# Optimization experiments

Hardware: AMD Instinct MI355X
Metric: run time of the kernel (lower is better)

Reference implementation:

```python
import jax, jax.numpy as jnp
import numpy as np

B = 8          # batch size (static)
GRID = 1024    # spatial grid H = W
PER = 25000    # active sites per batch item
N = B * PER

_OFFSETS = [(dx, dy) for dx in (-1, 0, 1) for dy in (-1, 0, 1)]  # 3x3 kernel


def _build_sparse_inputs():
    """Sample unique active 2D coords per batch item and build the 3x3
    submanifold neighbor map: nbr[i, k] = index of neighbor site at kernel
    offset k, or -1 if that coordinate is inactive."""
    rng = np.random.default_rng(0)
    bs, xs, ys = [], [], []
    for b in range(B):
        flat = rng.choice(GRID * GRID, size=PER, replace=False)
        bs.append(np.full(PER, b, np.int64))
        xs.append((flat // GRID).astype(np.int64))
        ys.append((flat % GRID).astype(np.int64))
    bb = np.concatenate(bs); xx = np.concatenate(xs); yy = np.concatenate(ys)
    # hash lookup table: (b, x, y) -> site index
    lut = np.full(B * GRID * GRID, -1, np.int64)
    lut[bb * GRID * GRID + xx * GRID + yy] = np.arange(N, dtype=np.int64)
    nbr = np.full((N, 9), -1, np.int64)
    for k, (dx, dy) in enumerate(_OFFSETS):
        nx, ny = xx + dx, yy + dy
        ok = (nx >= 0) & (nx < GRID) & (ny >= 0) & (ny < GRID)
        key = bb * GRID * GRID + np.clip(nx, 0, GRID - 1) * GRID + np.clip(ny, 0, GRID - 1)
        nbr[:, k] = np.where(ok, lut[key], -1)
    return bb, nbr


def setup_inputs() -> dict:
    key = jax.random.key(0)
    k1, k2, k3 = jax.random.split(key, 3)
    batch_np, nbr_np = _build_sparse_inputs()
    feats = jax.random.normal(k1, (N, 3), dtype=jnp.float32)
    # He (kaiming normal, relu): std = sqrt(2 / fan_in), fan_in = 9 * Cin
    W1 = jax.random.normal(k2, (9, 3, 256), dtype=jnp.float32) * np.sqrt(2.0 / (9 * 3))
    W2 = jax.random.normal(k3, (9, 256, 256), dtype=jnp.float32) * np.sqrt(2.0 / (9 * 256))
    return {
        "feats": feats,
        "W1": W1,
        "W2": W2,
        "nbr": jnp.asarray(nbr_np),
        "batch_ids": jnp.asarray(batch_np),
    }


def _subm_conv(feat, W, nbr):
    """Submanifold 3x3 conv: out[i] = sum_k feat[nbr[i,k]] @ W[k] over valid
    neighbors. feat: [N, Cin], W: [9, Cin, Cout], nbr: [N, 9] -> [N, Cout]."""
    out = jnp.zeros((feat.shape[0], W.shape[2]), dtype=feat.dtype)
    for k in range(9):  # fixed small kernel loop
        idx = nbr[:, k]
        valid = (idx >= 0).astype(feat.dtype)[:, None]
        g = feat[jnp.maximum(idx, 0)] * valid  # masked gather [N, Cin]
        out = out + g @ W[k]
    return out


def reference(feats, W1, W2, nbr, batch_ids):
    h = jax.nn.relu(_subm_conv(feats, W1, nbr))   # [N, 256]
    h = jax.nn.relu(_subm_conv(h, W2, nbr))       # [N, 256]
    # global average pool per batch item -> [B, 256]
    sums = jax.ops.segment_sum(h, batch_ids, num_segments=B)
    counts = jax.ops.segment_sum(jnp.ones((h.shape[0],), h.dtype), batch_ids, num_segments=B)
    return sums / counts[:, None]
```

## Files before the change

kernel.cpp:

```cpp
#include <hip/hip_runtime.h>
#include <hip/hip_bf16.h>

typedef __attribute__((ext_vector_type(8))) short bh8;
typedef __attribute__((ext_vector_type(4))) float f32x4;

#define NB 8
#define SLOTS 64
#define CAP 6144
#define CROWS 36864
#define CBLOCKS 512
#define FROWS 64
#define TSTRIDE 264

__device__ __forceinline__ void gld_lds16(const void* g, void* l) {
  __builtin_amdgcn_global_load_lds(
      (const __attribute__((address_space(1))) void*)g,
      (__attribute__((address_space(3))) void*)l, 16, 0, 0);
}

__device__ __forceinline__ unsigned short f2bu(float f) {
  union { __hip_bfloat16 h; unsigned short u; } cv;
  cv.h = __float2bfloat16(f);
  return cv.u;
}
__device__ __forceinline__ float bu2f(unsigned short u) {
  return __uint_as_float(((unsigned)u) << 16);
}

__global__ void w1t_kernel(const float* __restrict__ W1, short* __restrict__ w1bt) {
  const int n = threadIdx.x;
#pragma unroll
  for (int kk = 0; kk < 32; ++kk)
    w1bt[n * 32 + kk] = (kk < 27) ? (short)f2bu(W1[kk * 256 + n]) : (short)0;
}

__device__ __forceinline__ float3 ldf3(const float* __restrict__ f,
                                       const int* s_nbr, int idx) {
  int s = s_nbr[idx];
  long long sc = (s < 0) ? 0 : s;
  float3 r;
  r.x = f[3 * sc]; r.y = f[3 * sc + 1]; r.z = f[3 * sc + 2];
  if (s < 0) { r.x = 0.f; r.y = 0.f; r.z = 0.f; }
  return r;
}

__global__ __launch_bounds__(256, 2) void conv1_mfma_kernel(
    const float* __restrict__ feats, const short* __restrict__ w1bt,
    const int* __restrict__ nbr, __hip_bfloat16* __restrict__ h1b, int N) {
  __shared__ int s_nbr[64 * 9];
  __shared__ unsigned short tile[64 * TSTRIDE];
  const int tid = threadIdx.x;
  const int base = blockIdx.x * 64;

  for (int t = tid; t < 64 * 9; t += 256) s_nbr[t] = nbr[base * 9 + t];
  __syncthreads();

  const int wave = tid >> 6, lane = tid & 63;
  const int q = lane >> 4, m16 = lane & 15;
  const int rbase = (wave * 16 + m16) * 9;

  bh8 a;
  if (q == 0) {
    float3 t0 = ldf3(feats, s_nbr, rbase + 0);
    float3 t1 = ldf3(feats, s_nbr, rbase + 1);
    float3 t2 = ldf3(feats, s_nbr, rbase + 2);
    a[0] = (short)f2bu(t0.x); a[1] = (short)f2bu(t0.y); a[2] = (short)f2bu(t0.z);
    a[3] = (short)f2bu(t1.x); a[4] = (short)f2bu(t1.y); a[5] = (short)f2bu(t1.z);
    a[6] = (short)f2bu(t2.x); a[7] = (short)f2bu(t2.y);
  } else if (q == 1) {
    float3 t2 = ldf3(feats, s_nbr, rbase + 2);
    float3 t3 = ldf3(feats, s_nbr, rbase + 3);
    float3 t4 = ldf3(feats, s_nbr, rbase + 4);
    float3 t5 = ldf3(feats, s_nbr, rbase + 5);
    a[0] = (short)f2bu(t2.z);
    a[1] = (short)f2bu(t3.x); a[2] = (short)f2bu(t3.y); a[3] = (short)f2bu(t3.z);
    a[4] = (short)f2bu(t4.x); a[5] = (short)f2bu(t4.y); a[6] = (short)f2bu(t4.z);
    a[7] = (short)f2bu(t5.x);
  } else if (q == 2) {
    float3 t5 = ldf3(feats, s_nbr, rbase + 5);
    float3 t6 = ldf3(feats, s_nbr, rbase + 6);
    float3 t7 = ldf3(feats, s_nbr, rbase + 7);
    a[0] = (short)f2bu(t5.y); a[1] = (short)f2bu(t5.z);
    a[2] = (short)f2bu(t6.x); a[3] = (short)f2bu(t6.y); a[4] = (short)f2bu(t6.z);
    a[5] = (short)f2bu(t7.x); a[6] = (short)f2bu(t7.y); a[7] = (short)f2bu(t7.z);
  } else {
    float3 t8 = ldf3(feats, s_nbr, rbase + 8);
    a[0] = (short)f2bu(t8.x); a[1] = (short)f2bu(t8.y); a[2] = (short)f2bu(t8.z);
    a[3] = 0; a[4] = 0; a[5] = 0; a[6] = 0; a[7] = 0;
  }

  f32x4 acc[16];
#pragma unroll
  for (int nj = 0; nj < 16; ++nj) {
    bh8 b = *(const bh8*)(w1bt + (nj * 16 + m16) * 32 + q * 8);
    acc[nj] = __builtin_amdgcn_mfma_f32_16x16x32_bf16(a, b, (f32x4)0.f, 0, 0, 0);
  }

#pragma unroll
  for (int nj = 0; nj < 16; ++nj)
#pragma unroll
    for (int rr = 0; rr < 4; ++rr)
      tile[(wave * 16 + q * 4 + rr) * TSTRIDE + nj * 16 + m16] =
          f2bu(fmaxf(acc[nj][rr], 0.f));
  __syncthreads();

  {
    const int row = tid >> 2, seg = tid & 3;
    const int4* src = (const int4*)&tile[row * TSTRIDE + seg * 64];
    int4* dst = (int4*)(h1b + (long long)(base + row) * 256 + seg * 64);
#pragma unroll
    for (int i = 0; i < 8; ++i) dst[i] = src[i];
  }
}

__global__ __launch_bounds__(256) void w2t_kernel(
    const float* __restrict__ W2, __hip_bfloat16* __restrict__ w2bt) {
  __shared__ float tile[16][256];
  int k = blockIdx.x >> 4, t = blockIdx.x & 15;
  int tid = threadIdx.x;
#pragma unroll
  for (int r = 0; r < 16; ++r) tile[r][tid] = W2[k * 65536 + (t * 16 + r) * 256 + tid];
  __syncthreads();
#pragma unroll
  for (int r = 0; r < 16; ++r)
    w2bt[k * 65536 + tid * 256 + t * 16 + r] = __float2bfloat16(tile[r][tid]);
}

__global__ __launch_bounds__(256) void build_pairs_kernel(
    const int* __restrict__ nbr, const int* __restrict__ bid,
    int* __restrict__ nOff, int* __restrict__ cnt, float* __restrict__ bcnt,
    int* __restrict__ cidmap, int* __restrict__ crow,
    int* __restrict__ psrc, int* __restrict__ pcnt_cid,
    int* __restrict__ pairlist, int N) {
  __shared__ int l_cnt[10];
  __shared__ int l_base[10];
  __shared__ int l_bcnt[NB];
  const int tid = threadIdx.x;
  if (tid < 10) l_cnt[tid] = 0;
  if (tid < NB) l_bcnt[tid] = 0;
  __syncthreads();

  const int i = blockIdx.x * 256 + tid;
  const bool active = (i < N);
  int s[9];
  int kpos[9];
  int loc_cid = -1;
  if (active) {
#pragma unroll
    for (int k = 0; k < 9; ++k) s[k] = nbr[i * 9 + k];
    bool any = false;
#pragma unroll
    for (int k = 0; k < 9; ++k)
      if (k != 4 && s[k] >= 0) any = true;
    if (any) {
      loc_cid = atomicAdd(&l_cnt[9], 1);
#pragma unroll
      for (int k = 0; k < 9; ++k) {
        kpos[k] = -1;
        if (k != 4 && s[k] >= 0) kpos[k] = atomicAdd(&l_cnt[k], 1);
      }
    }
    atomicAdd(&l_bcnt[bid[i]], 1);
  }
  __syncthreads();

  if (tid < 9) l_base[tid] = (l_cnt[tid] > 0) ? atomicAdd(&cnt[tid], l_cnt[tid]) : 0;
  else if (tid == 9) l_base[9] = (l_cnt[9] > 0) ? atomicAdd(nOff, l_cnt[9]) : 0;
  if (tid >= 32 && tid < 32 + NB && l_bcnt[tid - 32] > 0)
    atomicAdd(&bcnt[tid - 32], (float)l_bcnt[tid - 32]);
  __syncthreads();

  if (active) {
    int cid = -1;
    if (loc_cid >= 0) {
      cid = l_base[9] + loc_cid;
      if (cid >= CROWS) cid = -1;
    }
    cidmap[i] = cid;
    if (cid >= 0) {
      crow[cid] = i;
#pragma unroll
      for (int k = 0; k < 9; ++k) {
        if (k == 4 || kpos[k] < 0 || s[k] < 0) continue;
        int pos = l_base[k] + kpos[k];
        if (pos < CAP) {
          psrc[k * CAP + pos] = s[k];
          int slot = atomicAdd(&pcnt_cid[cid], 1);
          if (slot < 8) pairlist[cid * 8 + slot] = k * CAP + pos;
        }
      }
    }
  }
}

__global__ __launch_bounds__(256, 2) void off_gemm_kernel(
    const __hip_bfloat16* __restrict__ h1, const __hip_bfloat16* __restrict__ w2bt,
    const int* __restrict__ cnt, const int* __restrict__ psrc,
    unsigned short* __restrict__ pout) {
  const int bpk = CAP / 64;
  int koff = blockIdx.x / bpk;
  int grp = blockIdx.x - koff * bpk;
  int k = koff + (koff >= 4 ? 1 : 0);
  int cntk = cnt[k];
  const int base = grp * 64;
  if (base >= cntk) return;

  __shared__ int s_src[64];
  const int tid = threadIdx.x;
  if (tid < 64) {
    int m = base + tid;
    s_src[tid] = (m < cntk) ? psrc[k * CAP + m] : 0;
  }

  const int wave = tid >> 6, lane = tid & 63, q = lane >> 4, m16 = lane & 15;
  const short* h1s = (const short*)h1;
  const short* wts = (const short*)w2bt + k * 65536;

  bh8 breg[4][8];
#pragma unroll
  for (int nj = 0; nj < 4; ++nj)
#pragma unroll
    for (int ko = 0; ko < 8; ++ko)
      breg[nj][ko] = *(const bh8*)(wts + (wave * 64 + nj * 16 + m16) * 256 + ko * 32 + q * 8);
  __syncthreads();

  bh8 aA[8];
  {
    const short* ap = h1s + (long long)s_src[m16] * 256 + q * 8;
#pragma unroll
    for (int ko = 0; ko < 8; ++ko) aA[ko] = *(const bh8*)(ap + ko * 32);
  }

#pragma unroll
  for (int t = 0; t < 4; ++t) {
    bh8 aN[8];
    if (t < 3) {
      const short* ap = h1s + (long long)s_src[(t + 1) * 16 + m16] * 256 + q * 8;
#pragma unroll
      for (int ko = 0; ko < 8; ++ko) aN[ko] = *(const bh8*)(ap + ko * 32);
    }
    f32x4 acc[4];
#pragma unroll
    for (int ko = 0; ko < 8; ++ko)
#pragma unroll
      for (int nj = 0; nj < 4; ++nj)
        acc[nj] = __builtin_amdgcn_mfma_f32_16x16x32_bf16(
            aA[ko], breg[nj][ko], (ko == 0) ? (f32x4)0.f : acc[nj], 0, 0, 0);
#pragma unroll
    for (int r = 0; r < 4; ++r) {
      int m = base + t * 16 + q * 4 + r;
      if (m >= cntk) continue;
      const long long rowb = (long long)(k * CAP + m) * 256;
#pragma unroll
      for (int nj = 0; nj < 4; ++nj)
        pout[rowb + wave * 64 + nj * 16 + m16] = f2bu(acc[nj][r]);
    }
#pragma unroll
    for (int ko = 0; ko < 8; ++ko) aA[ko] = aN[ko];
    if (base + (t + 1) * 16 >= cntk) break;
  }
}

__global__ __launch_bounds__(512, 2) void center_gemm_kernel(
    const __hip_bfloat16* __restrict__ h1, const __hip_bfloat16* __restrict__ w2bt,
    const int* __restrict__ cidmap, const int* __restrict__ bid,
    float* __restrict__ psums, unsigned short* __restrict__ h2cb, int N) {
  __shared__ __align__(16) short Abuf[2][64 * 256];

  const int tid = threadIdx.x;
  const int wave = tid >> 6, lane = tid & 63;
  const int q = lane >> 4, m16 = lane & 15;
  const int wc = wave << 5;
  const int slot = blockIdx.x & (SLOTS - 1);

  const short* h1s = (const short*)h1;
  const short* wts = (const short*)w2bt + 4 * 65536;

  bh8 breg[2][8];
#pragma unroll
  for (int nj = 0; nj < 2; ++nj)
#pragma unroll
    for (int ko = 0; ko < 8; ++ko)
      breg[nj][ko] = *(const bh8*)(wts + (wc + nj * 16 + m16) * 256 + ko * 32 + q * 8);

  const int nchunk = (N + 63) >> 6;
  const int span = (nchunk + CBLOCKS - 1) / CBLOCKS;
  const int c0 = blockIdx.x * span;
  if (c0 >= nchunk) return;
  int c1 = c0 + span;
  if (c1 > nchunk) c1 = nchunk;

  const int lrow = lane >> 5;
  const int jch  = lane & 31;

#define STAGE_CHUNK(cc, b)                                                     \
  {                                                                            \
    _Pragma("unroll") for (int t = 0; t < 4; ++t) {                            \
      int lr = (wave << 3) + (t << 1) + lrow;                                  \
      int g = ((cc) << 6) + lr;                                                \
      if (g >= N) g = N - 1;                                                   \
      int js = jch ^ (lr & 31);                                                \
      const short* src = h1s + (long long)g * 256 + (js << 3);                 \
      short* dst = &Abuf[b][((wave << 3) + (t << 1)) << 8];                    \
      gld_lds16((const void*)src, (void*)dst);                                 \
    }                                                                          \
  }

#define FLUSH_SACC()                                                           \
  if (cur_b0 >= 0) {                                                           \
    _Pragma("unroll") for (int lb = 0; lb < 2; ++lb) {                         \
      _Pragma("unroll") for (int nj = 0; nj < 2; ++nj) {                       \
        float v = sacc[lb][nj];                                                \
        v += __shfl_xor(v, 16, 64);                                            \
        v += __shfl_xor(v, 32, 64);                                            \
        if (q == 0 && v != 0.f) {                                              \
          int b = cur_b0 + lb;                                                 \
          if (b < NB)                                                          \
            atomicAdd(&psums[(slot * NB + b) * 256 + wc + nj * 16 + m16], v);  \
        }                                                                      \
      }                                                                        \
    }                                                                          \
  }

  STAGE_CHUNK(c0, 0);
  int cur = 0;
  int cur_b0 = -1;
  float sacc[2][2];
#pragma unroll
  for (int lb = 0; lb < 2; ++lb)
#pragma unroll
    for (int nj = 0; nj < 2; ++nj) sacc[lb][nj] = 0.f;

  for (int c = c0; c < c1; ++c) {
    __syncthreads();

    int4 bid4[4], cid4[4];
#pragma unroll
    for (int mi = 0; mi < 4; ++mi) {
      const int rb = (c << 6) + mi * 16 + q * 4;
      bid4[mi] = *(const int4*)(&bid[rb]);
      cid4[mi] = *(const int4*)(&cidmap[rb]);
    }
    const int b0 = bid[c << 6];

    if (c + 1 < c1) STAGE_CHUNK(c + 1, cur ^ 1);

    const short* Ab = &Abuf[cur][0];
    const short* abase[4];
    int xr[4];
#pragma unroll
    for (int mi = 0; mi < 4; ++mi) {
      int R = mi * 16 + m16;
      xr[mi] = R & 31;
      abase[mi] = Ab + (R << 8);
    }

    f32x4 acc[4][2];
#pragma unroll
    for (int ko = 0; ko < 8; ++ko) {
      bh8 a[4];
#pragma unroll
      for (int mi = 0; mi < 4; ++mi)
        a[mi] = *(const bh8*)(abase[mi] + (((ko * 4 + q) ^ xr[mi]) << 3));
#pragma unroll
      for (int mi = 0; mi < 4; ++mi)
#pragma unroll
        for (int nj = 0; nj < 2; ++nj)
          acc[mi][nj] = __builtin_amdgcn_mfma_f32_16x16x32_bf16(
              a[mi], breg[nj][ko], (ko == 0) ? (f32x4)0.f : acc[mi][nj], 0, 0, 0);
    }

    if (b0 != cur_b0) {
      FLUSH_SACC();
#pragma unroll
      for (int lb = 0; lb < 2; ++lb)
#pragma unroll
        for (int nj = 0; nj < 2; ++nj) sacc[lb][nj] = 0.f;
      cur_b0 = b0;
    }
#pragma unroll
    for (int mi = 0; mi < 4; ++mi) {
      const int bb[4] = {bid4[mi].x, bid4[mi].y, bid4[mi].z, bid4[mi].w};
      const int cc4[4] = {cid4[mi].x, cid4[mi].y, cid4[mi].z, cid4[mi].w};
      const int rb = (c << 6) + mi * 16 + q * 4;
#pragma unroll
      for (int rr = 0; rr < 4; ++rr) {
        if (rb + rr >= N) continue;
        if (cc4[rr] >= 0) {
          unsigned short* hp = h2cb + (long long)cc4[rr] * 256 + wc + m16;
          hp[0] = f2bu(acc[mi][0][rr]);
          hp[16] = f2bu(acc[mi][1][rr]);
          continue;
        }
        const int lb = (bb[rr] != b0) ? 1 : 0;
#pragma unroll
        for (int nj = 0; nj < 2; ++nj)
          sacc[lb][nj] += fmaxf(acc[mi][nj][rr], 0.f);
      }
    }

    cur ^= 1;
  }
  FLUSH_SACC();
#undef STAGE_CHUNK
#undef FLUSH_SACC
}

__global__ __launch_bounds__(256) void fixup_kernel(
    const unsigned short* __restrict__ h2cb, const unsigned short* __restrict__ pout,
    const int* __restrict__ pairlist, const int* __restrict__ pcnt_cid,
    const int* __restrict__ crow, const int* __restrict__ bid,
    const int* __restrict__ nOffp, float* __restrict__ psums) {
  __shared__ float lsum[NB * 256];
  __shared__ int s_b[FROWS], s_np[FROWS], s_pl[FROWS * 8];
  int nc = *nOffp;
  if (nc > CROWS) nc = CROWS;
  const int t0 = blockIdx.x * FROWS;
  if (t0 >= nc) return;
  const int tid = threadIdx.x;

  if (tid < FROWS) {
    int m = t0 + tid;
    bool v = (m < nc);
    s_b[tid] = v ? bid[crow[m]] : -1;
    int np = v ? pcnt_cid[m] : 0;
    s_np[tid] = (np > 8) ? 8 : np;
  }
  for (int i = tid; i < FROWS * 8; i += 256) {
    int m = t0 + (i >> 3);
    s_pl[i] = (m < nc) ? pairlist[m * 8 + (i & 7)] : 0;
  }
#pragma unroll
  for (int b = 0; b < NB; ++b) lsum[b * 256 + tid] = 0.f;
  __syncthreads();

  const int g = tid >> 6;
  const int cg = tid & 63;
  const ushort4* h2v = (const ushort4*)h2cb;
  const ushort4* pov = (const ushort4*)pout;

  float4 s0 = {0.f, 0.f, 0.f, 0.f}, s1 = {0.f, 0.f, 0.f, 0.f};
  const int r0 = g * 16;
  const int b0 = s_b[r0];
  int b1 = -1;
  for (int r = r0; r < r0 + 16; ++r) {
    const int b = s_b[r];
    if (b < 0) break;
    ushort4 u = h2v[(long long)(t0 + r) * 64 + cg];
    float4 x = {bu2f(u.x), bu2f(u.y), bu2f(u.z), bu2f(u.w)};
    const int np = s_np[r];
    for (int j = 0; j < np; ++j) {
      ushort4 p = pov[(long long)s_pl[r * 8 + j] * 64 + cg];
      x.x += bu2f(p.x); x.y += bu2f(p.y); x.z += bu2f(p.z); x.w += bu2f(p.w);
    }
    x.x = fmaxf(x.x, 0.f); x.y = fmaxf(x.y, 0.f);
    x.z = fmaxf(x.z, 0.f); x.w = fmaxf(x.w, 0.f);
    if (b == b0) {
      s0.x += x.x; s0.y += x.y; s0.z += x.z; s0.w += x.w;
    } else {
      b1 = b;
      s1.x += x.x; s1.y += x.y; s1.z += x.z; s1.w += x.w;
    }
  }
  if (b0 >= 0) {
    float* p0 = &lsum[b0 * 256 + cg * 4];
    atomicAdd(p0 + 0, s0.x); atomicAdd(p0 + 1, s0.y);
    atomicAdd(p0 + 2, s0.z); atomicAdd(p0 + 3, s0.w);
  }
  if (b1 >= 0 && b1 < NB) {
    float* p1 = &lsum[b1 * 256 + cg * 4];
    atomicAdd(p1 + 0, s1.x); atomicAdd(p1 + 1, s1.y);
    atomicAdd(p1 + 2, s1.z); atomicAdd(p1 + 3, s1.w);
  }
  __syncthreads();

  const int slot = blockIdx.x & (SLOTS - 1);
#pragma unroll
  for (int b = 0; b < NB; ++b) {
    float v = lsum[b * 256 + tid];
    if (v != 0.f) atomicAdd(&psums[(slot * NB + b) * 256 + tid], v);
  }
}

__global__ void finalize_kernel(const float* __restrict__ psums,
                                const float* __restrict__ bcnt,
                                float* __restrict__ out) {
  int b = blockIdx.x, c = threadIdx.x;
  float s = 0.f;
  for (int t = 0; t < SLOTS; ++t) s += psums[(t * NB + b) * 256 + c];
  out[b * 256 + c] = s / bcnt[b];
}

extern "C" void kernel_launch(void* const* d_in, const int* in_sizes, int n_in,
                              void* d_out, int out_size, void* d_ws, size_t ws_size,
                              hipStream_t stream) {
  const float* feats = (const float*)d_in[0];
  const float* W1    = (const float*)d_in[1];
  const float* W2    = (const float*)d_in[2];
  const int*   nbr   = (const int*)d_in[3];
  const int*   bid   = (const int*)d_in[4];
  float* out = (float*)d_out;
  const int N = in_sizes[0] / 3;

  char* ws = (char*)d_ws;
  size_t o = 0;
  float* psums = (float*)(ws + o); o += (size_t)SLOTS * NB * 256 * 4;
  float* bcnt  = (float*)(ws + o); o += NB * 4;
  int*   nOff  = (int*)(ws + o);   o += 4;
  int*   cnt   = (int*)(ws + o);   o += 9 * 4;
  o = (o + 255) & ~(size_t)255;
  int* pcnt_cid = (int*)(ws + o); o += (size_t)CROWS * 4;
  size_t zero1 = o;
  int* psrc = (int*)(ws + o); o += (size_t)9 * CAP * 4;
  int* pairlist = (int*)(ws + o); o += (size_t)CROWS * 8 * 4;
  int* cidmap = (int*)(ws + o); o += (size_t)N * 4;
  int* crow = (int*)(ws + o); o += (size_t)CROWS * 4;
  o = (o + 255) & ~(size_t)255;
  unsigned short* h2cb = (unsigned short*)(ws + o); o += (size_t)CROWS * 256 * 2;
  unsigned short* pout = (unsigned short*)(ws + o); o += (size_t)9 * CAP * 256 * 2;
  __hip_bfloat16* w2bt = (__hip_bfloat16*)(ws + o); o += (size_t)9 * 65536 * 2;
  short* w1bt = (short*)(ws + o); o += (size_t)256 * 32 * 2;
  __hip_bfloat16* h1b  = (__hip_bfloat16*)(ws + o); o += (size_t)N * 256 * 2;

  hipMemsetAsync(d_ws, 0, zero1, stream);

  w1t_kernel<<<1, 256, 0, stream>>>(W1, w1bt);
  conv1_mfma_kernel<<<(N + 63) / 64, 256, 0, stream>>>(feats, w1bt, nbr, h1b, N);
  w2t_kernel<<<9 * 16, 256, 0, stream>>>(W2, w2bt);
  build_pairs_kernel<<<(N + 255) / 256, 256, 0, stream>>>(
      nbr, bid, nOff, cnt, bcnt, cidmap, crow, psrc, pcnt_cid, pairlist, N);
  off_gemm_kernel<<<8 * (CAP / 64), 256, 0, stream>>>(h1b, w2bt, cnt, psrc, pout);
  center_gemm_kernel<<<CBLOCKS, 512, 0, stream>>>(h1b, w2bt, cidmap, bid, psums,
                                                  h2cb, N);
  fixup_kernel<<<(CROWS + FROWS - 1) / FROWS, 256, 0, stream>>>(
      h2cb, pout, pairlist, pcnt_cid, crow, bid, nOff, psums);
  finalize_kernel<<<NB, 256, 0, stream>>>(psums, bcnt, out);
}
```

Before: 271.6 us.

## Merge preprocessing and GEMM kernels into two heterogeneous phase kernels

Merges w1 transpose, conv1, w2 transpose and pair building into one phase1 kernel whose blocks pick their role from the block index, and merges the center and offset GEMMs into one phase2 kernel. Center rows that need fixup now get their center product from a separate gathered GEMM over crow instead of being written during the dense pass. Each conv1 block now converts W1 into LDS itself, and conv1 writes h1 directly without LDS staging. The goal is fewer launches and better overlap of the small kernels, at the cost of redundant W1 conversion, uncoalesced h1 stores, and a grid of mixed block types with different resource needs.

New measurement: 272.1 us. About the same (+0.2%).

```diff
diff --git a/kernel.cpp b/kernel.cpp
--- a/kernel.cpp
+++ b/kernel.cpp
@@ -8,9 +8,8 @@
 #define SLOTS 64
 #define CAP 6144
 #define CROWS 36864
-#define CBLOCKS 512
+#define CGB 256
 #define FROWS 64
-#define TSTRIDE 264
 
 __device__ __forceinline__ void gld_lds16(const void* g, void* l) {
   __builtin_amdgcn_global_load_lds(
@@ -27,271 +26,186 @@
   return __uint_as_float(((unsigned)u) << 16);
 }
 
-__global__ void w1t_kernel(const float* __restrict__ W1, short* __restrict__ w1bt) {
-  const int n = threadIdx.x;
-#pragma unroll
-  for (int kk = 0; kk < 32; ++kk)
-    w1bt[n * 32 + kk] = (kk < 27) ? (short)f2bu(W1[kk * 256 + n]) : (short)0;
-}
-
-__device__ __forceinline__ float3 ldf3(const float* __restrict__ f,
-                                       const int* s_nbr, int idx) {
-  int s = s_nbr[idx];
-  long long sc = (s < 0) ? 0 : s;
-  float3 r;
-  r.x = f[3 * sc]; r.y = f[3 * sc + 1]; r.z = f[3 * sc + 2];
-  if (s < 0) { r.x = 0.f; r.y = 0.f; r.z = 0.f; }
-  return r;
-}
-
-__global__ __launch_bounds__(256, 2) void conv1_mfma_kernel(
-    const float* __restrict__ feats, const short* __restrict__ w1bt,
-    const int* __restrict__ nbr, __hip_bfloat16* __restrict__ h1b, int N) {
-  __shared__ int s_nbr[64 * 9];
-  __shared__ unsigned short tile[64 * TSTRIDE];
+__global__ __launch_bounds__(256, 2) void phase1_kernel(
+    const float* __restrict__ feats, const float* __restrict__ W1,
+    const float* __restrict__ W2, const int* __restrict__ nbr,
+    const int* __restrict__ bid, __hip_bfloat16* __restrict__ h1b,
+    __hip_bfloat16* __restrict__ w2bt, int* __restrict__ nOff,
+    int* __restrict__ cnt, float* __restrict__ bcnt, int* __restrict__ cidmap,
+    int* __restrict__ crow, int* __restrict__ psrc, int* __restrict__ pcnt_cid,
+    int* __restrict__ pairlist, int N) {
+  __shared__ union {
+    struct { unsigned short w1s[256 * 32]; int s_nbr[64 * 9]; } c1;
+    struct { int l_cnt[10]; int l_base[10]; int l_bcnt[NB]; } bld;
+    struct { float tile[16][256]; } w2;
+  } sm;
+
+  const int nc1 = (N + 63) >> 6;
+  const int nbld = (N + 255) >> 8;
+  int bx = blockIdx.x;
   const int tid = threadIdx.x;
-  const int base = blockIdx.x * 64;
-
-  for (int t = tid; t < 64 * 9; t += 256) s_nbr[t] = nbr[base * 9 + t];
-  __syncthreads();
-
-  const int wave = tid >> 6, lane = tid & 63;
-  const int q = lane >> 4, m16 = lane & 15;
-  const int rbase = (wave * 16 + m16) * 9;
-
-  bh8 a;
-  if (q == 0) {
-    float3 t0 = ldf3(feats, s_nbr, rbase + 0);
-    float3 t1 = ldf3(feats, s_nbr, rbase + 1);
-    float3 t2 = ldf3(feats, s_nbr, rbase + 2);
-    a[0] = (short)f2bu(t0.x); a[1] = (short)f2bu(t0.y); a[2] = (short)f2bu(t0.z);
-    a[3] = (short)f2bu(t1.x); a[4] = (short)f2bu(t1.y); a[5] = (short)f2bu(t1.z);
-    a[6] = (short)f2bu(t2.x); a[7] = (short)f2bu(t2.y);
-  } else if (q == 1) {
-    float3 t2 = ldf3(feats, s_nbr, rbase + 2);
-    float3 t3 = ldf3(feats, s_nbr, rbase + 3);
-    float3 t4 = ldf3(feats, s_nbr, rbase + 4);
-    float3 t5 = ldf3(feats, s_nbr, rbase + 5);
-    a[0] = (short)f2bu(t2.z);
-    a[1] = (short)f2bu(t3.x); a[2] = (short)f2bu(t3.y); a[3] = (short)f2bu(t3.z);
-    a[4] = (short)f2bu(t4.x); a[5] = (short)f2bu(t4.y); a[6] = (short)f2bu(t4.z);
-    a[7] = (short)f2bu(t5.x);
-  } else if (q == 2) {
-    float3 t5 = ldf3(feats, s_nbr, rbase + 5);
-    float3 t6 = ldf3(feats, s_nbr, rbase + 6);
-    float3 t7 = ldf3(feats, s_nbr, rbase + 7);
-    a[0] = (short)f2bu(t5.y); a[1] = (short)f2bu(t5.z);
-    a[2] = (short)f2bu(t6.x); a[3] = (short)f2bu(t6.y); a[4] = (short)f2bu(t6.z);
-    a[5] = (short)f2bu(t7.x); a[6] = (short)f2bu(t7.y); a[7] = (short)f2bu(t7.z);
-  } else {
-    float3 t8 = ldf3(feats, s_nbr, rbase + 8);
-    a[0] = (short)f2bu(t8.x); a[1] = (short)f2bu(t8.y); a[2] = (short)f2bu(t8.z);
-    a[3] = 0; a[4] = 0; a[5] = 0; a[6] = 0; a[7] = 0;
-  }
-
-  f32x4 acc[16];
-#pragma unroll
-  for (int nj = 0; nj < 16; ++nj) {
-    bh8 b = *(const bh8*)(w1bt + (nj * 16 + m16) * 32 + q * 8);
-    acc[nj] = __builtin_amdgcn_mfma_f32_16x16x32_bf16(a, b, (f32x4)0.f, 0, 0, 0);
-  }
-
-#pragma unroll
-  for (int nj = 0; nj < 16; ++nj)
-#pragma unroll
-    for (int rr = 0; rr < 4; ++rr)
-      tile[(wave * 16 + q * 4 + rr) * TSTRIDE + nj * 16 + m16] =
-          f2bu(fmaxf(acc[nj][rr], 0.f));
-  __syncthreads();
+
+  if (bx < nc1) {
+    const int base = bx * 64;
+#pragma unroll 9
+    for (int kk = 0; kk < 27; ++kk)
+      sm.c1.w1s[tid * 32 + kk] = f2bu(W1[kk * 256 + tid]);
+#pragma unroll
+    for (int kk = 27; kk < 32; ++kk) sm.c1.w1s[tid * 32 + kk] = 0;
+    for (int t = tid; t < 64 * 9; t += 256) sm.c1.s_nbr[t] = nbr[base * 9 + t];
+    __syncthreads();
+
+    const int wave = tid >> 6, lane = tid & 63;
+    const int q = lane >> 4, m16 = lane & 15;
+    const int rbase = (wave * 16 + m16) * 9;
+    const int* s_nbr = sm.c1.s_nbr;
+
+    float v[9 * 3];
+    int t_lo[4] = {0, 2, 5, 8}, t_hi[4] = {3, 6, 8, 9};
+    for (int tt = t_lo[q]; tt < t_hi[q]; ++tt) {
+      int s = s_nbr[rbase + tt];
+      long long sc = (s < 0) ? 0 : s;
+      float x = feats[3 * sc], y = feats[3 * sc + 1], z = feats[3 * sc + 2];
+      if (s < 0) { x = 0.f; y = 0.f; z = 0.f; }
+      v[tt * 3 + 0] = x; v[tt * 3 + 1] = y; v[tt * 3 + 2] = z;
+    }
+    bh8 a;
+#pragma unroll
+    for (int j = 0; j < 8; ++j) {
+      int col = q * 8 + j;
+      a[j] = (col < 27) ? (short)f2bu(v[col]) : (short)0;
+    }
+
+    f32x4 acc[16];
+#pragma unroll
+    for (int nj = 0; nj < 16; ++nj) {
+      bh8 b = *(const bh8*)(&sm.c1.w1s[(nj * 16 + m16) * 32 + q * 8]);
+      acc[nj] = __builtin_amdgcn_mfma_f32_16x16x32_bf16(a, b, (f32x4)0.f, 0, 0, 0);
+    }
+    const int growb = base + wave * 16 + q * 4;
+#pragma unroll
+    for (int rr = 0; rr < 4; ++rr) {
+      __hip_bfloat16* rowp = h1b + (long long)(growb + rr) * 256 + m16;
+#pragma unroll
+      for (int nj = 0; nj < 16; ++nj)
+        rowp[nj * 16] = __float2bfloat16(fmaxf(acc[nj][rr], 0.f));
+    }
+    return;
+  }
+  bx -= nc1;
+
+  if (bx < nbld) {
+    if (tid < 10) sm.bld.l_cnt[tid] = 0;
+    if (tid < NB) sm.bld.l_bcnt[tid] = 0;
+    __syncthreads();
+
+    const int i = bx * 256 + tid;
+    const bool active = (i < N);
+    int s[9];
+    int kpos[9];
+    int loc_cid = -1;
+    if (active) {
+#pragma unroll
+      for (int k = 0; k < 9; ++k) s[k] = nbr[i * 9 + k];
+      bool any = false;
+#pragma unroll
+      for (int k = 0; k < 9; ++k)
+        if (k != 4 && s[k] >= 0) any = true;
+      if (any) {
+        loc_cid = atomicAdd(&sm.bld.l_cnt[9], 1);
+#pragma unroll
+        for (int k = 0; k < 9; ++k) {
+          kpos[k] = -1;
+          if (k != 4 && s[k] >= 0) kpos[k] = atomicAdd(&sm.bld.l_cnt[k], 1);
+        }
+      }
+      atomicAdd(&sm.bld.l_bcnt[bid[i]], 1);
+    }
+    __syncthreads();
+
+    if (tid < 9)
+      sm.bld.l_base[tid] =
+          (sm.bld.l_cnt[tid] > 0) ? atomicAdd(&cnt[tid], sm.bld.l_cnt[tid]) : 0;
+    else if (tid == 9)
+      sm.bld.l_base[9] = (sm.bld.l_cnt[9] > 0) ? atomicAdd(nOff, sm.bld.l_cnt[9]) : 0;
+    if (tid >= 32 && tid < 32 + NB && sm.bld.l_bcnt[tid - 32] > 0)
+      atomicAdd(&bcnt[tid - 32], (float)sm.bld.l_bcnt[tid - 32]);
+    __syncthreads();
+
+    if (active) {
+      int cid = -1;
+      if (loc_cid >= 0) {
+        cid = sm.bld.l_base[9] + loc_cid;
+        if (cid >= CROWS) cid = -1;
+      }
+      cidmap[i] = cid;
+      if (cid >= 0) {
+        crow[cid] = i;
+#pragma unroll
+        for (int k = 0; k < 9; ++k) {
+          if (k == 4 || kpos[k] < 0 || s[k] < 0) continue;
+          int pos = sm.bld.l_base[k] + kpos[k];
+          if (pos < CAP) {
+            psrc[k * CAP + pos] = s[k];
+            int slot = atomicAdd(&pcnt_cid[cid], 1);
+            if (slot < 8) pairlist[cid * 8 + slot] = k * CAP + pos;
+          }
+        }
+      }
+    }
+    return;
+  }
+  bx -= nbld;
 
   {
-    const int row = tid >> 2, seg = tid & 3;
-    const int4* src = (const int4*)&tile[row * TSTRIDE + seg * 64];
-    int4* dst = (int4*)(h1b + (long long)(base + row) * 256 + seg * 64);
-#pragma unroll
-    for (int i = 0; i < 8; ++i) dst[i] = src[i];
-  }
-}
-
-__global__ __launch_bounds__(256) void w2t_kernel(
-    const float* __restrict__ W2, __hip_bfloat16* __restrict__ w2bt) {
-  __shared__ float tile[16][256];
-  int k = blockIdx.x >> 4, t = blockIdx.x & 15;
-  int tid = threadIdx.x;
-#pragma unroll
-  for (int r = 0; r < 16; ++r) tile[r][tid] = W2[k * 65536 + (t * 16 + r) * 256 + tid];
-  __syncthreads();
-#pragma unroll
-  for (int r = 0; r < 16; ++r)
-    w2bt[k * 65536 + tid * 256 + t * 16 + r] = __float2bfloat16(tile[r][tid]);
-}
-
-__global__ __launch_bounds__(256) void build_pairs_kernel(
-    const int* __restrict__ nbr, const int* __restrict__ bid,
-    int* __restrict__ nOff, int* __restrict__ cnt, float* __restrict__ bcnt,
-    int* __restrict__ cidmap, int* __restrict__ crow,
-    int* __restrict__ psrc, int* __restrict__ pcnt_cid,
-    int* __restrict__ pairlist, int N) {
-  __shared__ int l_cnt[10];
-  __shared__ int l_base[10];
-  __shared__ int l_bcnt[NB];
-  const int tid = threadIdx.x;
-  if (tid < 10) l_cnt[tid] = 0;
-  if (tid < NB) l_bcnt[tid] = 0;
-  __syncthreads();
-
-  const int i = blockIdx.x * 256 + tid;
-  const bool active = (i < N);
-  int s[9];
-  int kpos[9];
-  int loc_cid = -1;
-  if (active) {
-#pragma unroll
-    for (int k = 0; k < 9; ++k) s[k] = nbr[i * 9 + k];
-    bool any = false;
-#pragma unroll
-    for (int k = 0; k < 9; ++k)
-      if (k != 4 && s[k] >= 0) any = true;
-    if (any) {
-      loc_cid = atomicAdd(&l_cnt[9], 1);
-#pragma unroll
-      for (int k = 0; k < 9; ++k) {
-        kpos[k] = -1;
-        if (k != 4 && s[k] >= 0) kpos[k] = atomicAdd(&l_cnt[k], 1);
-      }
-    }
-    atomicAdd(&l_bcnt[bid[i]], 1);
-  }
-  __syncthreads();
-
-  if (tid < 9) l_base[tid] = (l_cnt[tid] > 0) ? atomicAdd(&cnt[tid], l_cnt[tid]) : 0;
-  else if (tid == 9) l_base[9] = (l_cnt[9] > 0) ? atomicAdd(nOff, l_cnt[9]) : 0;
-  if (tid >= 32 && tid < 32 + NB && l_bcnt[tid - 32] > 0)
-    atomicAdd(&bcnt[tid - 32], (float)l_bcnt[tid - 32]);
-  __syncthreads();
-
-  if (active) {
-    int cid = -1;
-    if (loc_cid >= 0) {
-      cid = l_base[9] + loc_cid;
-      if (cid >= CROWS) cid = -1;
-    }
-    cidmap[i] = cid;
-    if (cid >= 0) {
-      crow[cid] = i;
-#pragma unroll
-      for (int k = 0; k < 9; ++k) {
-        if (k == 4 || kpos[k] < 0 || s[k] < 0) continue;
-        int pos = l_base[k] + kpos[k];
-        if (pos < CAP) {
-          psrc[k * CAP + pos] = s[k];
-          int slot = atomicAdd(&pcnt_cid[cid], 1);
-          if (slot < 8) pairlist[cid * 8 + slot] = k * CAP + pos;
-        }
-      }
-    }
-  }
-}
-
-__global__ __launch_bounds__(256, 2) void off_gemm_kernel(
-    const __hip_bfloat16* __restrict__ h1, const __hip_bfloat16* __restrict__ w2bt,
-    const int* __restrict__ cnt, const int* __restrict__ psrc,
-    unsigned short* __restrict__ pout) {
-  const int bpk = CAP / 64;
-  int koff = blockIdx.x / bpk;
-  int grp = blockIdx.x - koff * bpk;
-  int k = koff + (koff >= 4 ? 1 : 0);
-  int cntk = cnt[k];
-  const int base = grp * 64;
-  if (base >= cntk) return;
-
-  __shared__ int s_src[64];
-  const int tid = threadIdx.x;
-  if (tid < 64) {
-    int m = base + tid;
-    s_src[tid] = (m < cntk) ? psrc[k * CAP + m] : 0;
-  }
-
-  const int wave = tid >> 6, lane = tid & 63, q = lane >> 4, m16 = lane & 15;
-  const short* h1s = (const short*)h1;
-  const short* wts = (const short*)w2bt + k * 65536;
-
-  bh8 breg[4][8];
-#pragma unroll
-  for (int nj = 0; nj < 4; ++nj)
-#pragma unroll
-    for (int ko = 0; ko < 8; ++ko)
-      breg[nj][ko] = *(const bh8*)(wts + (wave * 64 + nj * 16 + m16) * 256 + ko * 32 + q * 8);
-  __syncthreads();
-
-  bh8 aA[8];
-  {
-    const short* ap = h1s + (long long)s_src[m16] * 256 + q * 8;
-#pragma unroll
-    for (int ko = 0; ko < 8; ++ko) aA[ko] = *(const bh8*)(ap + ko * 32);
-  }
-
-#pragma unroll
-  for (int t = 0; t < 4; ++t) {
-    bh8 aN[8];
-    if (t < 3) {
-      const short* ap = h1s + (long long)s_src[(t + 1) * 16 + m16] * 256 + q * 8;
-#pragma unroll
-      for (int ko = 0; ko < 8; ++ko) aN[ko] = *(const bh8*)(ap + ko * 32);
-    }
-    f32x4 acc[4];
-#pragma unroll
-    for (int ko = 0; ko < 8; ++ko)
-#pragma unroll
-      for (int nj = 0; nj < 4; ++nj)
-        acc[nj] = __builtin_amdgcn_mfma_f32_16x16x32_bf16(
-            aA[ko], breg[nj][ko], (ko == 0) ? (f32x4)0.f : acc[nj], 0, 0, 0);
-#pragma unroll
-    for (int r = 0; r < 4; ++r) {
-      int m = base + t * 16 + q * 4 + r;
-      if (m >= cntk) continue;
-      const long long rowb = (long long)(k * CAP + m) * 256;
-#pragma unroll
-      for (int nj = 0; nj < 4; ++nj)
-        pout[rowb + wave * 64 + nj * 16 + m16] = f2bu(acc[nj][r]);
-    }
-#pragma unroll
-    for (int ko = 0; ko < 8; ++ko) aA[ko] = aN[ko];
-    if (base + (t + 1) * 16 >= cntk) break;
-  }
-}
-
-__global__ __launch_bounds__(512, 2) void center_gemm_kernel(
+    int k = bx >> 4, t = bx & 15;
+#pragma unroll
+    for (int r = 0; r < 16; ++r)
+      sm.w2.tile[r][tid] = W2[k * 65536 + (t * 16 + r) * 256 + tid];
+    __syncthreads();
+#pragma unroll
+    for (int r = 0; r < 16; ++r)
+      w2bt[k * 65536 + tid * 256 + t * 16 + r] = __float2bfloat16(sm.w2.tile[r][tid]);
+  }
+}
+
+__global__ __launch_bounds__(512, 2) void phase2_kernel(
     const __hip_bfloat16* __restrict__ h1, const __hip_bfloat16* __restrict__ w2bt,
     const int* __restrict__ cidmap, const int* __restrict__ bid,
-    float* __restrict__ psums, unsigned short* __restrict__ h2cb, int N) {
+    const int* __restrict__ cnt, const int* __restrict__ psrc,
+    const int* __restrict__ nOffp, const int* __restrict__ crow,
+    float* __restrict__ psums, unsigned short* __restrict__ h2cb,
+    unsigned short* __restrict__ pout, int N) {
   __shared__ __align__(16) short Abuf[2][64 * 256];
 
+  int bx = blockIdx.x;
   const int tid = threadIdx.x;
   const int wave = tid >> 6, lane = tid & 63;
   const int q = lane >> 4, m16 = lane & 15;
-  const int wc = wave << 5;
-  const int slot = blockIdx.x & (SLOTS - 1);
-
   const short* h1s = (const short*)h1;
-  const short* wts = (const short*)w2bt + 4 * 65536;
-
-  bh8 breg[2][8];
-#pragma unroll
-  for (int nj = 0; nj < 2; ++nj)
-#pragma unroll
-    for (int ko = 0; ko < 8; ++ko)
-      breg[nj][ko] = *(const bh8*)(wts + (wc + nj * 16 + m16) * 256 + ko * 32 + q * 8);
-
-  const int nchunk = (N + 63) >> 6;
-  const int span = (nchunk + CBLOCKS - 1) / CBLOCKS;
-  const int c0 = blockIdx.x * span;
-  if (c0 >= nchunk) return;
-  int c1 = c0 + span;
-  if (c1 > nchunk) c1 = nchunk;
-
-  const int lrow = lane >> 5;
-  const int jch  = lane & 31;
+
+  if (bx < CGB) {
+    const int wc = wave << 5;
+    const int slot = bx & (SLOTS - 1);
+    const short* wts = (const short*)w2bt + 4 * 65536;
+
+    bh8 breg[2][8];
+#pragma unroll
+    for (int nj = 0; nj < 2; ++nj)
+#pragma unroll
+      for (int ko = 0; ko < 8; ++ko)
+        breg[nj][ko] =
+            *(const bh8*)(wts + (wc + nj * 16 + m16) * 256 + ko * 32 + q * 8);
+
+    const int nchunk = (N + 63) >> 6;
+    const int span = (nchunk + CGB - 1) / CGB;
+    const int c0 = bx * span;
+    if (c0 >= nchunk) return;
+    int c1 = c0 + span;
+    if (c1 > nchunk) c1 = nchunk;
+
+    const int lrow = lane >> 5;
+    const int jch = lane & 31;
 
 #define STAGE_CHUNK(cc, b)                                                     \
   {                                                                            \
@@ -322,88 +236,147 @@
     }                                                                          \
   }
 
-  STAGE_CHUNK(c0, 0);
-  int cur = 0;
-  int cur_b0 = -1;
-  float sacc[2][2];
-#pragma unroll
-  for (int lb = 0; lb < 2; ++lb)
-#pragma unroll
-    for (int nj = 0; nj < 2; ++nj) sacc[lb][nj] = 0.f;
-
-  for (int c = c0; c < c1; ++c) {
-    __syncthreads();
-
-    int4 bid4[4], cid4[4];
-#pragma unroll
-    for (int mi = 0; mi < 4; ++mi) {
-      const int rb = (c << 6) + mi * 16 + q * 4;
-      bid4[mi] = *(const int4*)(&bid[rb]);
-      cid4[mi] = *(const int4*)(&cidmap[rb]);
-    }
-    const int b0 = bid[c << 6];
-
-    if (c + 1 < c1) STAGE_CHUNK(c + 1, cur ^ 1);
-
-    const short* Ab = &Abuf[cur][0];
-    const short* abase[4];
-    int xr[4];
-#pragma unroll
-    for (int mi = 0; mi < 4; ++mi) {
-      int R = mi * 16 + m16;
-      xr[mi] = R & 31;
-      abase[mi] = Ab + (R << 8);
-    }
-
-    f32x4 acc[4][2];
-#pragma unroll
-    for (int ko = 0; ko < 8; ++ko) {
-      bh8 a[4];
-#pragma unroll
-      for (int mi = 0; mi < 4; ++mi)
-        a[mi] = *(const bh8*)(abase[mi] + (((ko * 4 + q) ^ xr[mi]) << 3));
-#pragma unroll
-      for (int mi = 0; mi < 4; ++mi)
-#pragma unroll
-        for (int nj = 0; nj < 2; ++nj)
-          acc[mi][nj] = __builtin_amdgcn_mfma_f32_16x16x32_bf16(
-              a[mi], breg[nj][ko], (ko == 0) ? (f32x4)0.f : acc[mi][nj], 0, 0, 0);
-    }
-
-    if (b0 != cur_b0) {
-      FLUSH_SACC();
-#pragma unroll
-      for (int lb = 0; lb < 2; ++lb)
-#pragma unroll
-        for (int nj = 0; nj < 2; ++nj) sacc[lb][nj] = 0.f;
-      cur_b0 = b0;
-    }
-#pragma unroll
-    for (int mi = 0; mi < 4; ++mi) {
-      const int bb[4] = {bid4[mi].x, bid4[mi].y, bid4[mi].z, bid4[mi].w};
-      const int cc4[4] = {cid4[mi].x, cid4[mi].y, cid4[mi].z, cid4[mi].w};
-      const int rb = (c << 6) + mi * 16 + q * 4;
-#pragma unroll
-      for (int rr = 0; rr < 4; ++rr) {
-        if (rb + rr >= N) continue;
-        if (cc4[rr] >= 0) {
-          unsigned short* hp = h2cb + (long long)cc4[rr] * 256 + wc + m16;
-          hp[0] = f2bu(acc[mi][0][rr]);
-          hp[16] = f2bu(acc[mi][1][rr]);
-          continue;
+    STAGE_CHUNK(c0, 0);
+    int cur = 0;
+    int cur_b0 = -1;
+    float sacc[2][2];
+#pragma unroll
+    for (int lb = 0; lb < 2; ++lb)
+#pragma unroll
+      for (int nj = 0; nj < 2; ++nj) sacc[lb][nj] = 0.f;
+
+    for (int c = c0; c < c1; ++c) {
+      __syncthreads();
+
+      int4 bid4[4], cid4[4];
+#pragma unroll
+      for (int mi = 0; mi < 4; ++mi) {
+        const int rb = (c << 6) + mi * 16 + q * 4;
+        bid4[mi] = *(const int4*)(&bid[rb]);
+        cid4[mi] = *(const int4*)(&cidmap[rb]);
+      }
+      const int b0 = bid[c << 6];
+
+      if (c + 1 < c1) STAGE_CHUNK(c + 1, cur ^ 1);
+
+      const short* Ab = &Abuf[cur][0];
+      const short* abase[4];
+      int xr[4];
+#pragma unroll
+      for (int mi = 0; mi < 4; ++mi) {
+        int R = mi * 16 + m16;
+        xr[mi] = R & 31;
+        abase[mi] = Ab + (R << 8);
+      }
+
+      f32x4 acc[4][2];
+#pragma unroll
+      for (int ko = 0; ko < 8; ++ko) {
+        bh8 a[4];
+#pragma unroll
+        for (int mi = 0; mi < 4; ++mi)
+          a[mi] = *(const bh8*)(abase[mi] + (((ko * 4 + q) ^ xr[mi]) << 3));
+#pragma unroll
+        for (int mi = 0; mi < 4; ++mi)
+#pragma unroll
+          for (int nj = 0; nj < 2; ++nj)
+            acc[mi][nj] = __builtin_amdgcn_mfma_f32_16x16x32_bf16(
+                a[mi], breg[nj][ko], (ko == 0) ? (f32x4)0.f : acc[mi][nj], 0, 0, 0);
+      }
+
+      if (b0 != cur_b0) {
+        FLUSH_SACC();
+#pragma unroll
+        for (int lb = 0; lb < 2; ++lb)
+#pragma unroll
+          for (int nj = 0; nj < 2; ++nj) sacc[lb][nj] = 0.f;
+        cur_b0 = b0;
+      }
+#pragma unroll
+      for (int mi = 0; mi < 4; ++mi) {
+        const int bb[4] = {bid4[mi].x, bid4[mi].y, bid4[mi].z, bid4[mi].w};
+        const int cc4[4] = {cid4[mi].x, cid4[mi].y, cid4[mi].z, cid4[mi].w};
+        const int rb = (c << 6) + mi * 16 + q * 4;
+#pragma unroll
+        for (int rr = 0; rr < 4; ++rr) {
+          if (rb + rr >= N) continue;
+          if (cc4[rr] >= 0) continue;
+          const int lb = (bb[rr] != b0) ? 1 : 0;
+#pragma unroll
+          for (int nj = 0; nj < 2; ++nj)
+            sacc[lb][nj] += fmaxf(acc[mi][nj][rr], 0.f);
         }
-        const int lb = (bb[rr] != b0) ? 1 : 0;
-#pragma unroll
-        for (int nj = 0; nj < 2; ++nj)
-          sacc[lb][nj] += fmaxf(acc[mi][nj][rr], 0.f);
-      }
-    }
-
-    cur ^= 1;
-  }
-  FLUSH_SACC();
+      }
+      cur ^= 1;
+    }
+    FLUSH_SACC();
 #undef STAGE_CHUNK
 #undef FLUSH_SACC
+    return;
+  }
+  bx -= CGB;
+
+  int* s_src = (int*)&Abuf[0][0];
+  const int OFFG = 8 * (CAP / 64);
+  int k = 4;
+  int gbase, cmax;
+  bool isoff;
+  if (bx < OFFG) {
+    int koff = bx / (CAP / 64);
+    int grp = bx - koff * (CAP / 64);
+    k = koff + (koff >= 4 ? 1 : 0);
+    cmax = cnt[k];
+    gbase = grp * 64;
+    isoff = true;
+  } else {
+    bx -= OFFG;
+    cmax = *nOffp;
+    if (cmax > CROWS) cmax = CROWS;
+    gbase = bx * 64;
+    isoff = false;
+  }
+  if (gbase >= cmax) return;
+
+  if (tid < 64) {
+    int m = gbase + tid;
+    s_src[tid] = (m < cmax) ? (isoff ? psrc[k * CAP + m] : crow[m]) : 0;
+  }
+  const short* wts = (const short*)w2bt + k * 65536;
+  const int wc = wave << 5;
+
+  bh8 breg[2][8];
+#pragma unroll
+  for (int nj = 0; nj < 2; ++nj)
+#pragma unroll
+    for (int ko = 0; ko < 8; ++ko)
+      breg[nj][ko] = *(const bh8*)(wts + (wc + nj * 16 + m16) * 256 + ko * 32 + q * 8);
+  __syncthreads();
+
+  for (int t = 0; t < 4; ++t) {
+    if (gbase + t * 16 >= cmax) break;
+    bh8 aA[8];
+    {
+      const short* ap = h1s + (long long)s_src[t * 16 + m16] * 256 + q * 8;
+#pragma unroll
+      for (int ko = 0; ko < 8; ++ko) aA[ko] = *(const bh8*)(ap + ko * 32);
+    }
+    f32x4 acc[2];
+#pragma unroll
+    for (int ko = 0; ko < 8; ++ko)
+#pragma unroll
+      for (int nj = 0; nj < 2; ++nj)
+        acc[nj] = __builtin_amdgcn_mfma_f32_16x16x32_bf16(
+            aA[ko], breg[nj][ko], (ko == 0) ? (f32x4)0.f : acc[nj], 0, 0, 0);
+#pragma unroll
+    for (int r = 0; r < 4; ++r) {
+      int m = gbase + t * 16 + q * 4 + r;
+      if (m >= cmax) continue;
+      unsigned short* dst =
+          isoff ? (pout + (long long)(k * CAP + m) * 256) : (h2cb + (long long)m * 256);
+      dst[wc + m16] = f2bu(acc[0][r]);
+      dst[wc + 16 + m16] = f2bu(acc[1][r]);
+    }
+  }
 }
 
 __global__ __launch_bounds__(256) void fixup_kernel(
@@ -519,19 +492,17 @@
   unsigned short* h2cb = (unsigned short*)(ws + o); o += (size_t)CROWS * 256 * 2;
   unsigned short* pout = (unsigned short*)(ws + o); o += (size_t)9 * CAP * 256 * 2;
   __hip_bfloat16* w2bt = (__hip_bfloat16*)(ws + o); o += (size_t)9 * 65536 * 2;
-  short* w1bt = (short*)(ws + o); o += (size_t)256 * 32 * 2;
   __hip_bfloat16* h1b  = (__hip_bfloat16*)(ws + o); o += (size_t)N * 256 * 2;
 
   hipMemsetAsync(d_ws, 0, zero1, stream);
 
-  w1t_kernel<<<1, 256, 0, stream>>>(W1, w1bt);
-  conv1_mfma_kernel<<<(N + 63) / 64, 256, 0, stream>>>(feats, w1bt, nbr, h1b, N);
-  w2t_kernel<<<9 * 16, 256, 0, stream>>>(W2, w2bt);
-  build_pairs_kernel<<<(N + 255) / 256, 256, 0, stream>>>(
-      nbr, bid, nOff, cnt, bcnt, cidmap, crow, psrc, pcnt_cid, pairlist, N);
-  off_gemm_kernel<<<8 * (CAP / 64), 256, 0, stream>>>(h1b, w2bt, cnt, psrc, pout);
-  center_gemm_kernel<<<CBLOCKS, 512, 0, stream>>>(h1b, w2bt, cidmap, bid, psums,
-                                                  h2cb, N);
+  const int nc1 = (N + 63) / 64;
+  const int nbld = (N + 255) / 256;
+  phase1_kernel<<<nc1 + nbld + 144, 256, 0, stream>>>(
+      feats, W1, W2, nbr, bid, h1b, w2bt, nOff, cnt, bcnt, cidmap, crow, psrc,
+      pcnt_cid, pairlist, N);
+  phase2_kernel<<<CGB + 8 * (CAP / 64) + CROWS / 64, 512, 0, stream>>>(
+      h1b, w2bt, cidmap, bid, cnt, psrc, nOff, crow, psums, h2cb, pout, N);
   fixup_kernel<<<(CROWS + FROWS - 1) / FROWS, 256, 0, stream>>>(
       h2cb, pout, pairlist, pcnt_cid, crow, bid, nOff, psums);
   finalize_kernel<<<NB, 256, 0, stream>>>(psums, bcnt, out);
```
